# Optimization experiments

Measured on AMD Instinct MI355X. Metric: run time of the kernel, lower is better.

The kernel has to match this reference:

```python
import jax, jax.numpy as jnp
import numpy as np

D_MODEL = 1024
HEADS = 16
DEPTH = D_MODEL // HEADS
B, S = 4, 4096
EPS_K = 1e-6  # kernel feature epsilon
EPS_LN = 1e-6


def setup_inputs() -> dict:
    key = jax.random.key(0)
    ks = jax.random.split(key, 8)
    lecun = 1.0 / np.sqrt(D_MODEL)  # LecunNormal stddev
    glorot = np.sqrt(2.0 / (D_MODEL + D_MODEL))  # keras Dense default
    return {
        "q": jax.random.normal(ks[0], (B, S, D_MODEL), jnp.float32),
        "k": jax.random.normal(ks[1], (B, S, D_MODEL), jnp.float32),
        "v": jax.random.normal(ks[2], (B, S, D_MODEL), jnp.float32),
        "mask": jnp.ones((B, S), jnp.float32),
        "wq": jax.random.normal(ks[3], (D_MODEL, D_MODEL), jnp.float32) * lecun,
        "wk": jax.random.normal(ks[4], (D_MODEL, D_MODEL), jnp.float32) * lecun,
        "wv": jax.random.normal(ks[5], (D_MODEL, D_MODEL), jnp.float32) * lecun,
        "ln_gamma": jnp.ones((D_MODEL,), jnp.float32),
        "ln_beta": jnp.zeros((D_MODEL,), jnp.float32),
        "dense_w": jax.random.normal(ks[6], (D_MODEL, D_MODEL), jnp.float32) * glorot,
        "dense_b": jnp.zeros((D_MODEL,), jnp.float32),
    }


def _layernorm(x, g, b):
    m = jnp.mean(x, axis=-1, keepdims=True)
    var = jnp.var(x, axis=-1, keepdims=True)
    return (x - m) * jax.lax.rsqrt(var + EPS_LN) * g + b


def _split_heads(x):
    bsz, sl, _ = x.shape
    return x.reshape(bsz, sl, HEADS, DEPTH).transpose(0, 2, 1, 3)  # [B,H,S,depth]


def reference(q, k, v, mask, wq, wk, wv, ln_gamma, ln_beta, dense_w, dense_b):
    bsz = q.shape[0]
    em = mask[:, None, :, None]  # [B,1,S,1] broadcast over heads/depth
    qh = _split_heads(_layernorm(q @ wq, ln_gamma, ln_beta))
    kh = _split_heads(_layernorm(k @ wk, ln_gamma, ln_beta))
    vh = _split_heads(_layernorm(v @ wv, ln_gamma, ln_beta))
    q_prime = jax.nn.relu(qh) + EPS_K
    k_prime = (jax.nn.relu(kh) + EPS_K) * em
    vh = vh * em
    kv = jnp.einsum('bhnd,bhne->bhde', k_prime, vh)  # [B,H,depth,depth]
    z = 1.0 / (jnp.einsum('bhnd,bhd->bhn', q_prime, k_prime.sum(axis=-2)) + EPS_K)
    att = jnp.einsum('bhnd,bhde,bhn->bhne', q_prime, kv, z)  # [B,H,S,depth]
    # Faithful to original: reshape WITHOUT transposing heads back.
    att = att.reshape(bsz, -1, D_MODEL)  # [B,S,d_model]
    out = att @ dense_w + dense_b
    return _layernorm(out, ln_gamma, ln_beta)
```

## Files before the change

kernel.cpp:

```cpp
#include <hip/hip_runtime.h>
#include <hip/hip_bf16.h>
#include <stdint.h>

#define D_MODEL 1024
#define S_LEN   4096
#define BATCH   4
#define HEADS   16
#define DEPTH   64
#define ROWS    (BATCH*S_LEN)
#define EPS_K_F 1e-6f
#define EPS_LN_F 1e-6f

typedef __attribute__((ext_vector_type(8))) short short8;
typedef __attribute__((ext_vector_type(4))) float f32x4;

__device__ __forceinline__ unsigned short f2bf(float f) {
  union { float f; unsigned u; } x; x.f = f;
  unsigned r = x.u + 0x7FFF + ((x.u >> 16) & 1);
  return (unsigned short)(r >> 16);
}
__device__ __forceinline__ float bf2f(unsigned short b) {
  union { unsigned u; float f; } x; x.u = ((unsigned)b) << 16;
  return x.f;
}
__device__ __forceinline__ void gload16(const void* g, void* l) {
  __builtin_amdgcn_global_load_lds(
      (const __attribute__((address_space(1))) void*)g,
      (__attribute__((address_space(3))) void*)l, 16, 0, 0);
}

__global__ __launch_bounds__(256) void cvt_f32_bf16_k(
    const float* __restrict__ in, unsigned short* __restrict__ out, int n4) {
  int i = blockIdx.x * 256 + threadIdx.x;
  if (i < n4) {
    float4 v = ((const float4*)in)[i];
    ushort4 o;
    o.x = f2bf(v.x); o.y = f2bf(v.y); o.z = f2bf(v.z); o.w = f2bf(v.w);
    ((ushort4*)out)[i] = o;
  }
}

__global__ __launch_bounds__(256) void wtrans_k(
    const float* __restrict__ W, unsigned short* __restrict__ Wt) {
  __shared__ float tile[32][33];
  int n0 = blockIdx.x * 32, k0 = blockIdx.y * 32;
  int tx = threadIdx.x & 31, ty = threadIdx.x >> 5;
  #pragma unroll
  for (int i = 0; i < 32; i += 8)
    tile[ty + i][tx] = W[(size_t)(k0 + ty + i) * D_MODEL + n0 + tx];
  __syncthreads();
  #pragma unroll
  for (int i = 0; i < 32; i += 8)
    Wt[(size_t)(n0 + ty + i) * D_MODEL + k0 + tx] = f2bf(tile[tx][ty + i]);
}


#define GEMM_EPILOGUE(HASBIAS)                                               \
  if (HASBIAS) {                                                             \
    float bv[4];                                                             \
    _Pragma("unroll")                                                        \
    for (int n = 0; n < 4; ++n)                                              \
      bv[n] = bias[(int)n0 + wcn * 64 + n * 16 + l15];                       \
    _Pragma("unroll")                                                        \
    for (int m = 0; m < 8; ++m)                                              \
      _Pragma("unroll")                                                      \
      for (int n = 0; n < 4; ++n)                                            \
        _Pragma("unroll")                                                    \
        for (int j = 0; j < 4; ++j)                                          \
          acc[m][n][j] += bv[n];                                             \
  }                                                                          \
  int seg = (int)(n0 >> 6) + wcn;                                            \
  _Pragma("unroll")                                                          \
  for (int m = 0; m < 8; ++m) {                                              \
    float s[4], s2[4];                                                       \
    _Pragma("unroll")                                                        \
    for (int j = 0; j < 4; ++j) {                                            \
      float a = 0.f, b = 0.f;                                                \
      _Pragma("unroll")                                                      \
      for (int n = 0; n < 4; ++n) { float x = acc[m][n][j]; a += x; b += x*x; } \
      s[j] = a; s2[j] = b;                                                   \
    }                                                                        \
    _Pragma("unroll")                                                        \
    for (int off = 1; off < 16; off <<= 1) {                                 \
      _Pragma("unroll")                                                      \
      for (int j = 0; j < 4; ++j) {                                          \
        s[j]  += __shfl_xor(s[j],  off);                                     \
        s2[j] += __shfl_xor(s2[j], off);                                     \
      }                                                                      \
    }                                                                        \
    if (l15 == 0) {                                                          \
      _Pragma("unroll")                                                      \
      for (int j = 0; j < 4; ++j) {                                          \
        int rg = (int)m0 + wr * 128 + m * 16 + lhi * 4 + j;                  \
        psum[rg * 16 + seg] = s[j];                                          \
        psq [rg * 16 + seg] = s2[j];                                         \
      }                                                                      \
    }                                                                        \
  }                                                                          \
  _Pragma("unroll")                                                          \
  for (int m = 0; m < 8; ++m)                                                \
    _Pragma("unroll")                                                        \
    for (int j = 0; j < 4; ++j) {                                            \
      size_t row = m0 + wr * 128 + m * 16 + lhi * 4 + j;                     \
      _Pragma("unroll")                                                      \
      for (int n = 0; n < 4; ++n) {                                          \
        int col = (int)n0 + wcn * 64 + n * 16 + l15;                         \
        Cb[row * N + col] = f2bf(acc[m][n][j]);                              \
      }                                                                      \
    }

#define GEMM_COMPUTE_TILE(ABUF, BBUF)                                        \
  _Pragma("unroll")                                                          \
  for (int kk = 0; kk < 2; ++kk) {                                           \
    short8 bfr[4];                                                           \
    _Pragma("unroll")                                                        \
    for (int n = 0; n < 4; ++n) {                                            \
      int rr = wcn * 64 + n * 16 + l15;                                      \
      int cx = (kk * 4 + lhi) ^ (l15 & 7);                                   \
      bfr[n] = *(const short8*)&(BBUF)[rr * 64 + cx * 8];                    \
    }                                                                        \
    _Pragma("unroll")                                                        \
    for (int mh = 0; mh < 2; ++mh) {                                         \
      short8 af[4];                                                          \
      _Pragma("unroll")                                                      \
      for (int m = 0; m < 4; ++m) {                                          \
        int rr = wr * 128 + (mh * 4 + m) * 16 + l15;                         \
        int cx = (kk * 4 + lhi) ^ (l15 & 7);                                 \
        af[m] = *(const short8*)&(ABUF)[rr * 64 + cx * 8];                   \
      }                                                                      \
      asm volatile("s_waitcnt lgkmcnt(0)" ::: "memory");                     \
      __builtin_amdgcn_sched_barrier(0);                                     \
      __builtin_amdgcn_s_setprio(1);                                         \
      _Pragma("unroll")                                                      \
      for (int m = 0; m < 4; ++m)                                            \
        _Pragma("unroll")                                                    \
        for (int n = 0; n < 4; ++n)                                          \
          acc[mh * 4 + m][n] = __builtin_amdgcn_mfma_f32_16x16x32_bf16(      \
              af[m], bfr[n], acc[mh * 4 + m][n], 0, 0, 0);                   \
      __builtin_amdgcn_s_setprio(0);                                         \
    }                                                                        \
  }

__global__ __launch_bounds__(512, 2) void gemm_bt_k(
    const unsigned short* __restrict__ A,
    const unsigned short* __restrict__ Bt,
    unsigned short* __restrict__ Cb,
    float* __restrict__ psum, float* __restrict__ psq,
    const float* __restrict__ bias,
    const float* __restrict__ side_src,
    unsigned short* __restrict__ side_dst,
    int M, int N, int K) {
  __shared__ unsigned short Al[2][256 * 64];
  __shared__ unsigned short Bl[2][256 * 64];
  int t = threadIdx.x;
  int lane = t & 63, wid = t >> 6;
  int wr = wid >> 2, wcn = wid & 3;
  int l15 = lane & 15, lhi = lane >> 4;
  int p = blockIdx.x;
  int cb = (p >> 3) & 3;
  int rb = (p & 7) | ((p >> 5) << 3);
  size_t m0 = (size_t)rb * 256, n0 = (size_t)cb * 256;
  f32x4 acc[8][4] = {};

  const int KT = K >> 6;

#define STAGE_AB(kof_, buf_) do {                                            \
    _Pragma("unroll")                                                        \
    for (int sub = 0; sub < 4; ++sub) {                                      \
      int idx = sub * 512 + t; int r_ = idx >> 3, cl_ = idx & 7;             \
      int cg_ = cl_ ^ (r_ & 7);                                              \
      gload16(A + (m0 + r_) * (size_t)K + (kof_) + cg_ * 8,                  \
              &Al[buf_][idx * 8]);                                           \
    }                                                                        \
    _Pragma("unroll")                                                        \
    for (int sub = 0; sub < 4; ++sub) {                                      \
      int idx = sub * 512 + t; int r_ = idx >> 3, cl_ = idx & 7;             \
      int cg_ = cl_ ^ (r_ & 7);                                              \
      gload16(Bt + (n0 + r_) * (size_t)K + (kof_) + cg_ * 8,                 \
              &Bl[buf_][idx * 8]);                                           \
    }                                                                        \
  } while (0)

  float4 sreg0 = {}, sreg1 = {};
  size_t sbase = (size_t)p * 65536 + (size_t)t * 8;

  STAGE_AB(0, 0);
  if (side_dst) {
    sreg0 = *(const float4*)(side_src + sbase);
    sreg1 = *(const float4*)(side_src + sbase + 4);
  }
  asm volatile("s_waitcnt vmcnt(0)" ::: "memory");
  __builtin_amdgcn_s_barrier();
  __builtin_amdgcn_sched_barrier(0);

  for (int kt = 0; kt < KT; ++kt) {
    int buf = kt & 1;
    if (kt + 1 < KT) STAGE_AB((kt + 1) << 6, buf ^ 1);
    if (side_dst) {
      uint4 pk;
      pk.x = (unsigned)f2bf(sreg0.x) | ((unsigned)f2bf(sreg0.y) << 16);
      pk.y = (unsigned)f2bf(sreg0.z) | ((unsigned)f2bf(sreg0.w) << 16);
      pk.z = (unsigned)f2bf(sreg1.x) | ((unsigned)f2bf(sreg1.y) << 16);
      pk.w = (unsigned)f2bf(sreg1.z) | ((unsigned)f2bf(sreg1.w) << 16);
      *(uint4*)(side_dst + sbase + (size_t)kt * 4096) = pk;
      if (kt + 1 < KT) {
        const float* sp = side_src + sbase + (size_t)(kt + 1) * 4096;
        sreg0 = *(const float4*)sp;
        sreg1 = *(const float4*)(sp + 4);
      }
    }
    __builtin_amdgcn_sched_barrier(0);
    GEMM_COMPUTE_TILE(Al[buf], Bl[buf]);
    asm volatile("s_waitcnt vmcnt(0) lgkmcnt(0)" ::: "memory");
    __builtin_amdgcn_s_barrier();
    __builtin_amdgcn_sched_barrier(0);
  }
#undef STAGE_AB

  GEMM_EPILOGUE(bias != nullptr)
}

__global__ __launch_bounds__(256) void ln_act_k(
    const unsigned short* __restrict__ Cb,
    const float* __restrict__ psum, const float* __restrict__ psq,
    const float* __restrict__ gamma, const float* __restrict__ beta,
    const float* __restrict__ mask,
    unsigned short* __restrict__ out, int mode) {
  int row = blockIdx.x;
  int t = threadIdx.x;
  float s = 0.f, s2 = 0.f;
  #pragma unroll
  for (int i = 0; i < 16; ++i) { s += psum[row * 16 + i]; s2 += psq[row * 16 + i]; }
  float mean = s * (1.f / D_MODEL);
  float var = s2 * (1.f / D_MODEL) - mean * mean;
  float rstd = rsqrtf(var + EPS_LN_F);
  float mk = (mode > 0) ? mask[row] : 1.f;
  ushort4 cv = ((const ushort4*)(Cb + (size_t)row * D_MODEL))[t];
  float4 gv = ((const float4*)gamma)[t];
  float4 bv = ((const float4*)beta)[t];
  float av[4] = {bf2f(cv.x), bf2f(cv.y), bf2f(cv.z), bf2f(cv.w)};
  float g4[4] = {gv.x, gv.y, gv.z, gv.w};
  float b4[4] = {bv.x, bv.y, bv.z, bv.w};
  unsigned short ov[4];
  #pragma unroll
  for (int j = 0; j < 4; ++j) {
    float ln = (av[j] - mean) * rstd * g4[j] + b4[j];
    if (mode == 0)      ln = fmaxf(ln, 0.f) + EPS_K_F;
    else if (mode == 1) ln = (fmaxf(ln, 0.f) + EPS_K_F) * mk;
    else                ln = ln * mk;
    ov[j] = f2bf(ln);
  }
  ushort4 o; o.x = ov[0]; o.y = ov[1]; o.z = ov[2]; o.w = ov[3];
  ((ushort4*)(out + (size_t)row * D_MODEL))[t] = o;
}

__global__ __launch_bounds__(256) void ln_final_k(
    const unsigned short* __restrict__ Cb,
    const float* __restrict__ psum, const float* __restrict__ psq,
    const float* __restrict__ gamma, const float* __restrict__ beta,
    float* __restrict__ out) {
  int row = blockIdx.x;
  int t = threadIdx.x;
  float s = 0.f, s2 = 0.f;
  #pragma unroll
  for (int i = 0; i < 16; ++i) { s += psum[row * 16 + i]; s2 += psq[row * 16 + i]; }
  float mean = s * (1.f / D_MODEL);
  float var = s2 * (1.f / D_MODEL) - mean * mean;
  float rstd = rsqrtf(var + EPS_LN_F);
  ushort4 cv = ((const ushort4*)(Cb + (size_t)row * D_MODEL))[t];
  float4 gv = ((const float4*)gamma)[t];
  float4 bv = ((const float4*)beta)[t];
  float4 w;
  w.x = (bf2f(cv.x) - mean) * rstd * gv.x + bv.x;
  w.y = (bf2f(cv.y) - mean) * rstd * gv.y + bv.y;
  w.z = (bf2f(cv.z) - mean) * rstd * gv.z + bv.z;
  w.w = (bf2f(cv.w) - mean) * rstd * gv.w + bv.w;
  ((float4*)(out + (size_t)row * D_MODEL))[t] = w;
}

__global__ __launch_bounds__(256) void kv_mfma_k(
    const unsigned short* __restrict__ Kp, const unsigned short* __restrict__ Vp,
    float* __restrict__ part, float* __restrict__ kspart) {
  __shared__ unsigned short Kl[4096];
  __shared__ unsigned short Vl[4096];
  int bh = blockIdx.y, chunk = blockIdx.x;
  int b_ = bh >> 4, h = bh & 15;
  int t = threadIdx.x, lane = t & 63, w = t >> 6;
  int l15 = lane & 15, g = lane >> 4;

  int sn = t >> 2, sd16 = t & 3;
  int sc = sd16 ^ ((sn >> 3) & 3);
  size_t goff = (size_t)sn * D_MODEL + h * DEPTH + sd16 * 16;
  int ldst = sn * 64 + sc * 16;

  short8 ones;
  #pragma unroll
  for (int i = 0; i < 8; ++i) ones[i] = (short)0x3F80;

  f32x4 acc[4] = {};
  f32x4 ks = {};

  int baseA = ((w ^ g) << 4) + l15;
  int baseB0 = ((0 ^ g) << 4) + l15;
  int baseB1 = ((1 ^ g) << 4) + l15;
  int baseB2 = ((2 ^ g) << 4) + l15;
  int baseB3 = ((3 ^ g) << 4) + l15;

  size_t rowbase = ((size_t)b_ * S_LEN + (size_t)chunk * 512) * D_MODEL;
  for (int tile = 0; tile < 8; ++tile) {
    const unsigned short* kg = Kp + rowbase + (size_t)tile * 64 * D_MODEL + goff;
    const unsigned short* vg = Vp + rowbase + (size_t)tile * 64 * D_MODEL + goff;
    uint4 ra = *(const uint4*)kg;
    uint4 rb = *(const uint4*)(kg + 8);
    uint4 rc = *(const uint4*)vg;
    uint4 rd = *(const uint4*)(vg + 8);
    __syncthreads();
    *(uint4*)&Kl[ldst]     = ra;
    *(uint4*)&Kl[ldst + 8] = rb;
    *(uint4*)&Vl[ldst]     = rc;
    *(uint4*)&Vl[ldst + 8] = rd;
    __syncthreads();
    #pragma unroll
    for (int kk = 0; kk < 2; ++kk) {
      int nb = (kk * 32 + g * 8) * 64;
      short8 af, bf0, bf1, bf2, bf3;
      #pragma unroll
      for (int i = 0; i < 8; ++i) {
        int rowoff = nb + i * 64;
        af[i]  = (short)Kl[rowoff + baseA];
        bf0[i] = (short)Vl[rowoff + baseB0];
        bf1[i] = (short)Vl[rowoff + baseB1];
        bf2[i] = (short)Vl[rowoff + baseB2];
        bf3[i] = (short)Vl[rowoff + baseB3];
      }
      acc[0] = __builtin_amdgcn_mfma_f32_16x16x32_bf16(af, bf0, acc[0], 0, 0, 0);
      acc[1] = __builtin_amdgcn_mfma_f32_16x16x32_bf16(af, bf1, acc[1], 0, 0, 0);
      acc[2] = __builtin_amdgcn_mfma_f32_16x16x32_bf16(af, bf2, acc[2], 0, 0, 0);
      acc[3] = __builtin_amdgcn_mfma_f32_16x16x32_bf16(af, bf3, acc[3], 0, 0, 0);
      ks     = __builtin_amdgcn_mfma_f32_16x16x32_bf16(af, ones, ks, 0, 0, 0);
    }
  }
  float* pp = part + ((size_t)bh * 8 + chunk) * 4096;
  #pragma unroll
  for (int nf = 0; nf < 4; ++nf)
    #pragma unroll
    for (int r = 0; r < 4; ++r)
      pp[(16 * w + 4 * g + r) * 64 + 16 * nf + l15] = acc[nf][r];
  if (l15 == 0) {
    #pragma unroll
    for (int r = 0; r < 4; ++r)
      kspart[((size_t)bh * 8 + chunk) * 64 + 16 * w + 4 * g + r] = ks[r];
  }
}

__global__ __launch_bounds__(256) void kv_reduce_k(
    const float* __restrict__ part, const float* __restrict__ kspart,
    unsigned short* __restrict__ KVT, float* __restrict__ ksum) {
  int bh = blockIdx.x, t = threadIdx.x;
  for (int idx = t; idx < 4096; idx += 256) {
    int d = idx >> 6, e = idx & 63;
    float s = 0.f;
    #pragma unroll
    for (int c = 0; c < 8; ++c)
      s += part[((size_t)bh * 8 + c) * 4096 + d * 64 + e];
    KVT[(size_t)bh * 4096 + e * 64 + d] = f2bf(s);
  }
  if (t < 64) {
    float s = 0.f;
    #pragma unroll
    for (int c = 0; c < 8; ++c) s += kspart[((size_t)bh * 8 + c) * 64 + t];
    ksum[bh * 64 + t] = s;
  }
}

__global__ __launch_bounds__(256) void att_k(
    const unsigned short* __restrict__ Qp, const unsigned short* __restrict__ KVT,
    const float* __restrict__ ksum, unsigned short* __restrict__ att) {
  __shared__ unsigned short Ql[128 * 64];
  __shared__ unsigned short Kl[64 * 64];
  __shared__ float ksl[64];
  __shared__ float zl[128];
  int bh = blockIdx.y;
  int b = bh >> 4, h = bh & 15;
  int r0 = blockIdx.x * 128;
  int t = threadIdx.x, lane = t & 63, wid = t >> 6;
  int l15 = lane & 15, lhi = lane >> 4;
  #pragma unroll
  for (int i = 0; i < 4; ++i) {
    int cid = i * 256 + t;
    int r = cid >> 3, c8 = cid & 7;
    gload16(Qp + ((size_t)(b * S_LEN + r0 + r)) * D_MODEL + h * DEPTH + c8 * 8,
            &Ql[cid * 8]);
  }
  #pragma unroll
  for (int i = 0; i < 2; ++i) {
    int cid = i * 256 + t;
    gload16(KVT + (size_t)bh * 4096 + cid * 8, &Kl[cid * 8]);
  }
  if (t < 64) ksl[t] = ksum[bh * 64 + t];
  asm volatile("s_waitcnt vmcnt(0)" ::: "memory");
  __syncthreads();
  {
    int r = t >> 1, half = t & 1;
    float s = 0.f;
    #pragma unroll
    for (int j = 0; j < 32; ++j)
      s += bf2f(Ql[r * 64 + half * 32 + j]) * ksl[half * 32 + j];
    s += __shfl_xor(s, 1);
    if (half == 0) zl[r] = 1.f / (s + EPS_K_F);
  }
  __syncthreads();
  f32x4 acc[2][4] = {};
  #pragma unroll
  for (int kk = 0; kk < 2; ++kk) {
    short8 af[2], bfr[4];
    #pragma unroll
    for (int m = 0; m < 2; ++m)
      af[m] = *(const short8*)&Ql[(wid * 32 + m * 16 + l15) * 64 + kk * 32 + lhi * 8];
    #pragma unroll
    for (int n = 0; n < 4; ++n)
      bfr[n] = *(const short8*)&Kl[(n * 16 + l15) * 64 + kk * 32 + lhi * 8];
    #pragma unroll
    for (int m = 0; m < 2; ++m)
      #pragma unroll
      for (int n = 0; n < 4; ++n)
        acc[m][n] = __builtin_amdgcn_mfma_f32_16x16x32_bf16(af[m], bfr[n], acc[m][n], 0, 0, 0);
  }
  #pragma unroll
  for (int m = 0; m < 2; ++m)
    #pragma unroll
    for (int j = 0; j < 4; ++j) {
      int rl = wid * 32 + m * 16 + lhi * 4 + j;
      int n = r0 + rl;
      float z = zl[rl];
      #pragma unroll
      for (int nf = 0; nf < 4; ++nf) {
        int ee = nf * 16 + l15;
        size_t orow = (size_t)b * S_LEN + h * 256 + (n >> 4);
        int ocol = (n & 15) * 64 + ee;
        att[orow * D_MODEL + ocol] = f2bf(acc[m][nf][j] * z);
      }
    }
}

extern "C" void kernel_launch(void* const* d_in, const int* in_sizes, int n_in,
                              void* d_out, int out_size, void* d_ws, size_t ws_size,
                              hipStream_t stream) {
  (void)in_sizes; (void)n_in; (void)out_size; (void)ws_size;
  const float* q     = (const float*)d_in[0];
  const float* k     = (const float*)d_in[1];
  const float* v     = (const float*)d_in[2];
  const float* mask  = (const float*)d_in[3];
  const float* wq    = (const float*)d_in[4];
  const float* wk    = (const float*)d_in[5];
  const float* wv    = (const float*)d_in[6];
  const float* gamma = (const float*)d_in[7];
  const float* beta  = (const float*)d_in[8];
  const float* dw    = (const float*)d_in[9];
  const float* db    = (const float*)d_in[10];
  float* out = (float*)d_out;

  char* ws = (char*)d_ws;
  unsigned short* bufA = (unsigned short*)(ws);
  unsigned short* Qp   = (unsigned short*)(ws + 33554432);
  unsigned short* bufB = (unsigned short*)(ws + 67108864);
  unsigned short* Kp   = bufB;
  unsigned short* Vp   = (unsigned short*)(ws + 100663296);
  unsigned short* WqT  = (unsigned short*)(ws + 134217728);
  unsigned short* WkT = WqT + 1048576;
  unsigned short* WvT = WkT + 1048576;
  unsigned short* WdT = WvT + 1048576;
  float* part   = (float*)(ws);
  float* kspart = (float*)(ws + 8388608);
  unsigned short* KVT = (unsigned short*)(ws + 142606336);
  float* ksum = (float*)(ws + 143130624);
  float* psum = (float*)(ws + 143654912);
  float* psq  = (float*)(ws + 144703488);
  unsigned short* Cqkv = (unsigned short*)d_out;
  unsigned short* Cd   = Qp;

  dim3 b256(256);
  dim3 b512(512);
  int n4 = ROWS * D_MODEL / 4;
  dim3 cvtg(n4 / 256);
  dim3 wtg(32, 32);
  dim3 gemmg(256);
  dim3 lng(ROWS);

  wtrans_k<<<wtg, b256, 0, stream>>>(wq, WqT);
  wtrans_k<<<wtg, b256, 0, stream>>>(wk, WkT);
  wtrans_k<<<wtg, b256, 0, stream>>>(wv, WvT);
  wtrans_k<<<wtg, b256, 0, stream>>>(dw, WdT);

  cvt_f32_bf16_k<<<cvtg, b256, 0, stream>>>(q, bufA, n4);

  gemm_bt_k<<<gemmg, b512, 0, stream>>>(bufA, WqT, Cqkv, psum, psq, nullptr,
                                        k, bufB, ROWS, D_MODEL, D_MODEL);
  ln_act_k<<<lng, b256, 0, stream>>>(Cqkv, psum, psq, gamma, beta, nullptr, Qp, 0);

  gemm_bt_k<<<gemmg, b512, 0, stream>>>(bufB, WkT, Cqkv, psum, psq, nullptr,
                                        v, bufA, ROWS, D_MODEL, D_MODEL);
  ln_act_k<<<lng, b256, 0, stream>>>(Cqkv, psum, psq, gamma, beta, mask, Kp, 1);

  gemm_bt_k<<<gemmg, b512, 0, stream>>>(bufA, WvT, Cqkv, psum, psq, nullptr,
                                        nullptr, nullptr, ROWS, D_MODEL, D_MODEL);
  ln_act_k<<<lng, b256, 0, stream>>>(Cqkv, psum, psq, gamma, beta, mask, Vp, 2);

  kv_mfma_k<<<dim3(8, 64), b256, 0, stream>>>(Kp, Vp, part, kspart);
  kv_reduce_k<<<dim3(64), b256, 0, stream>>>(part, kspart, KVT, ksum);
  att_k<<<dim3(32, 64), b256, 0, stream>>>(Qp, KVT, ksum, bufA);

  gemm_bt_k<<<gemmg, b512, 0, stream>>>(bufA, WdT, Cd, psum, psq, db,
                                        nullptr, nullptr, ROWS, D_MODEL, D_MODEL);
  ln_final_k<<<lng, b256, 0, stream>>>(Cd, psum, psq, gamma, beta, out);
}
```

Baseline: 352.5 us.

## Replace double-buffered LDS staging with single buffer in GEMM kernel

```diff
diff --git a/kernel.cpp b/kernel.cpp
--- a/kernel.cpp
+++ b/kernel.cpp
@@ -150,8 +150,8 @@
     const float* __restrict__ side_src,
     unsigned short* __restrict__ side_dst,
     int M, int N, int K) {
-  __shared__ unsigned short Al[2][256 * 64];
-  __shared__ unsigned short Bl[2][256 * 64];
+  __shared__ unsigned short Al[256 * 64];
+  __shared__ unsigned short Bl[256 * 64];
   int t = threadIdx.x;
   int lane = t & 63, wid = t >> 6;
   int wr = wid >> 2, wcn = wid & 3;
@@ -164,58 +164,55 @@
 
   const int KT = K >> 6;
 
-#define STAGE_AB(kof_, buf_) do {                                            \
+#define STAGE_AB(kof_) do {                                                  \
     _Pragma("unroll")                                                        \
     for (int sub = 0; sub < 4; ++sub) {                                      \
       int idx = sub * 512 + t; int r_ = idx >> 3, cl_ = idx & 7;             \
       int cg_ = cl_ ^ (r_ & 7);                                              \
-      gload16(A + (m0 + r_) * (size_t)K + (kof_) + cg_ * 8,                  \
-              &Al[buf_][idx * 8]);                                           \
+      gload16(A + (m0 + r_) * (size_t)K + (kof_) + cg_ * 8, &Al[idx * 8]);   \
     }                                                                        \
     _Pragma("unroll")                                                        \
     for (int sub = 0; sub < 4; ++sub) {                                      \
       int idx = sub * 512 + t; int r_ = idx >> 3, cl_ = idx & 7;             \
       int cg_ = cl_ ^ (r_ & 7);                                              \
-      gload16(Bt + (n0 + r_) * (size_t)K + (kof_) + cg_ * 8,                 \
-              &Bl[buf_][idx * 8]);                                           \
+      gload16(Bt + (n0 + r_) * (size_t)K + (kof_) + cg_ * 8, &Bl[idx * 8]);  \
     }                                                                        \
   } while (0)
 
   float4 sreg0 = {}, sreg1 = {};
   size_t sbase = (size_t)p * 65536 + (size_t)t * 8;
 
-  STAGE_AB(0, 0);
-  if (side_dst) {
-    sreg0 = *(const float4*)(side_src + sbase);
-    sreg1 = *(const float4*)(side_src + sbase + 4);
-  }
-  asm volatile("s_waitcnt vmcnt(0)" ::: "memory");
-  __builtin_amdgcn_s_barrier();
-  __builtin_amdgcn_sched_barrier(0);
-
   for (int kt = 0; kt < KT; ++kt) {
-    int buf = kt & 1;
-    if (kt + 1 < KT) STAGE_AB((kt + 1) << 6, buf ^ 1);
+    STAGE_AB(kt << 6);
     if (side_dst) {
-      uint4 pk;
-      pk.x = (unsigned)f2bf(sreg0.x) | ((unsigned)f2bf(sreg0.y) << 16);
-      pk.y = (unsigned)f2bf(sreg0.z) | ((unsigned)f2bf(sreg0.w) << 16);
-      pk.z = (unsigned)f2bf(sreg1.x) | ((unsigned)f2bf(sreg1.y) << 16);
-      pk.w = (unsigned)f2bf(sreg1.z) | ((unsigned)f2bf(sreg1.w) << 16);
-      *(uint4*)(side_dst + sbase + (size_t)kt * 4096) = pk;
-      if (kt + 1 < KT) {
-        const float* sp = side_src + sbase + (size_t)(kt + 1) * 4096;
-        sreg0 = *(const float4*)sp;
-        sreg1 = *(const float4*)(sp + 4);
+      if (kt > 0) {
+        uint4 pk;
+        pk.x = (unsigned)f2bf(sreg0.x) | ((unsigned)f2bf(sreg0.y) << 16);
+        pk.y = (unsigned)f2bf(sreg0.z) | ((unsigned)f2bf(sreg0.w) << 16);
+        pk.z = (unsigned)f2bf(sreg1.x) | ((unsigned)f2bf(sreg1.y) << 16);
+        pk.w = (unsigned)f2bf(sreg1.z) | ((unsigned)f2bf(sreg1.w) << 16);
+        *(uint4*)(side_dst + sbase + (size_t)(kt - 1) * 4096) = pk;
       }
+      const float* sp = side_src + sbase + (size_t)kt * 4096;
+      sreg0 = *(const float4*)sp;
+      sreg1 = *(const float4*)(sp + 4);
     }
-    __builtin_amdgcn_sched_barrier(0);
-    GEMM_COMPUTE_TILE(Al[buf], Bl[buf]);
-    asm volatile("s_waitcnt vmcnt(0) lgkmcnt(0)" ::: "memory");
+    asm volatile("s_waitcnt vmcnt(0)" ::: "memory");
     __builtin_amdgcn_s_barrier();
     __builtin_amdgcn_sched_barrier(0);
+    GEMM_COMPUTE_TILE(Al, Bl);
+    __builtin_amdgcn_s_barrier();
+    __builtin_amdgcn_sched_barrier(0);
   }
 #undef STAGE_AB
+  if (side_dst) {
+    uint4 pk;
+    pk.x = (unsigned)f2bf(sreg0.x) | ((unsigned)f2bf(sreg0.y) << 16);
+    pk.y = (unsigned)f2bf(sreg0.z) | ((unsigned)f2bf(sreg0.w) << 16);
+    pk.z = (unsigned)f2bf(sreg1.x) | ((unsigned)f2bf(sreg1.y) << 16);
+    pk.w = (unsigned)f2bf(sreg1.z) | ((unsigned)f2bf(sreg1.w) << 16);
+    *(uint4*)(side_dst + sbase + (size_t)(KT - 1) * 4096) = pk;
+  }
 
   GEMM_EPILOGUE(bias != nullptr)
 }
```

Measured after the change: 366.2 us. 1.04x slower.

## Restructure GEMM mainloop into half-K stages with deeper prefetch; batch input conversions

Applied to the files above, without the earlier changes.

```diff
diff --git a/kernel.cpp b/kernel.cpp
--- a/kernel.cpp
+++ b/kernel.cpp
@@ -29,15 +29,19 @@
       (__attribute__((address_space(3))) void*)l, 16, 0, 0);
 }
 
-__global__ __launch_bounds__(256) void cvt_f32_bf16_k(
-    const float* __restrict__ in, unsigned short* __restrict__ out, int n4) {
-  int i = blockIdx.x * 256 + threadIdx.x;
-  if (i < n4) {
-    float4 v = ((const float4*)in)[i];
-    ushort4 o;
-    o.x = f2bf(v.x); o.y = f2bf(v.y); o.z = f2bf(v.z); o.w = f2bf(v.w);
-    ((ushort4*)out)[i] = o;
-  }
+__global__ __launch_bounds__(256) void cvt3_k(
+    const float* __restrict__ q, const float* __restrict__ k,
+    const float* __restrict__ v,
+    unsigned short* __restrict__ xq, unsigned short* __restrict__ xk,
+    unsigned short* __restrict__ xv, int nb_per) {
+  int tb = blockIdx.x / nb_per;
+  int i = (blockIdx.x % nb_per) * 256 + threadIdx.x;
+  const float* src = (tb == 0) ? q : (tb == 1) ? k : v;
+  unsigned short* dst = (tb == 0) ? xq : (tb == 1) ? xk : xv;
+  float4 val = ((const float4*)src)[i];
+  ushort4 o;
+  o.x = f2bf(val.x); o.y = f2bf(val.y); o.z = f2bf(val.z); o.w = f2bf(val.w);
+  ((ushort4*)dst)[i] = o;
 }
 
 __global__ __launch_bounds__(256) void wtrans_k(
@@ -109,37 +113,47 @@
       }                                                                      \
     }
 
-#define GEMM_COMPUTE_TILE(ABUF, BBUF)                                        \
-  _Pragma("unroll")                                                          \
-  for (int kk = 0; kk < 2; ++kk) {                                           \
-    short8 bfr[4];                                                           \
+#define STAGE_HALF(kof_, slot_, h_) do {                                     \
+    _Pragma("unroll")                                                        \
+    for (int j = 0; j < 2; ++j) {                                            \
+      int idx = j * 512 + t; int r_ = idx >> 2; int cs_ = idx & 3;           \
+      int c_ = cs_ ^ (r_ & 3);                                               \
+      gload16(A + (m0 + r_) * (size_t)K + (kof_) + (h_) * 32 + c_ * 8,       \
+              &Al[slot_][(h_) * 8192 + idx * 8]);                            \
+    }                                                                        \
+    _Pragma("unroll")                                                        \
+    for (int j = 0; j < 2; ++j) {                                            \
+      int idx = j * 512 + t; int r_ = idx >> 2; int cs_ = idx & 3;           \
+      int c_ = cs_ ^ (r_ & 3);                                               \
+      gload16(Bt + (n0 + r_) * (size_t)K + (kof_) + (h_) * 32 + c_ * 8,      \
+              &Bl[slot_][(h_) * 8192 + idx * 8]);                            \
+    }                                                                        \
+  } while (0)
+
+#define PH_READ_B(kk_)                                                       \
     _Pragma("unroll")                                                        \
     for (int n = 0; n < 4; ++n) {                                            \
-      int rr = wcn * 64 + n * 16 + l15;                                      \
-      int cx = (kk * 4 + lhi) ^ (l15 & 7);                                   \
-      bfr[n] = *(const short8*)&(BBUF)[rr * 64 + cx * 8];                    \
-    }                                                                        \
-    _Pragma("unroll")                                                        \
-    for (int mh = 0; mh < 2; ++mh) {                                         \
-      short8 af[4];                                                          \
+      int rb_ = wcn * 64 + n * 16 + l15;                                     \
+      bfr[n] = *(const short8*)&Bl[slot][(kk_) * 8192 + rb_ * 32 + cswz];    \
+    }
+#define PH_READ_A(kk_, mh_)                                                  \
+    _Pragma("unroll")                                                        \
+    for (int m = 0; m < 4; ++m) {                                            \
+      int ra_ = wr * 128 + ((mh_) * 4 + m) * 16 + l15;                       \
+      af[m] = *(const short8*)&Al[slot][(kk_) * 8192 + ra_ * 32 + cswz];     \
+    }
+#define PH_MFMA(mh_)                                                         \
+    __builtin_amdgcn_s_setprio(1);                                           \
+    _Pragma("unroll")                                                        \
+    for (int m = 0; m < 4; ++m)                                              \
       _Pragma("unroll")                                                      \
-      for (int m = 0; m < 4; ++m) {                                          \
-        int rr = wr * 128 + (mh * 4 + m) * 16 + l15;                         \
-        int cx = (kk * 4 + lhi) ^ (l15 & 7);                                 \
-        af[m] = *(const short8*)&(ABUF)[rr * 64 + cx * 8];                   \
-      }                                                                      \
-      asm volatile("s_waitcnt lgkmcnt(0)" ::: "memory");                     \
-      __builtin_amdgcn_sched_barrier(0);                                     \
-      __builtin_amdgcn_s_setprio(1);                                         \
-      _Pragma("unroll")                                                      \
-      for (int m = 0; m < 4; ++m)                                            \
-        _Pragma("unroll")                                                    \
-        for (int n = 0; n < 4; ++n)                                          \
-          acc[mh * 4 + m][n] = __builtin_amdgcn_mfma_f32_16x16x32_bf16(      \
-              af[m], bfr[n], acc[mh * 4 + m][n], 0, 0, 0);                   \
-      __builtin_amdgcn_s_setprio(0);                                         \
-    }                                                                        \
-  }
+      for (int n = 0; n < 4; ++n)                                            \
+        acc[(mh_) * 4 + m][n] = __builtin_amdgcn_mfma_f32_16x16x32_bf16(     \
+            af[m], bfr[n], acc[(mh_) * 4 + m][n], 0, 0, 0);                  \
+    __builtin_amdgcn_s_setprio(0);
+#define LGKM0                                                                \
+    asm volatile("s_waitcnt lgkmcnt(0)" ::: "memory");                       \
+    __builtin_amdgcn_sched_barrier(0);
 
 __global__ __launch_bounds__(512, 2) void gemm_bt_k(
     const unsigned short* __restrict__ A,
@@ -147,15 +161,14 @@
     unsigned short* __restrict__ Cb,
     float* __restrict__ psum, float* __restrict__ psq,
     const float* __restrict__ bias,
-    const float* __restrict__ side_src,
-    unsigned short* __restrict__ side_dst,
     int M, int N, int K) {
-  __shared__ unsigned short Al[2][256 * 64];
-  __shared__ unsigned short Bl[2][256 * 64];
+  __shared__ unsigned short Al[2][16384];
+  __shared__ unsigned short Bl[2][16384];
   int t = threadIdx.x;
   int lane = t & 63, wid = t >> 6;
   int wr = wid >> 2, wcn = wid & 3;
   int l15 = lane & 15, lhi = lane >> 4;
+  const int cswz = (lhi ^ (l15 & 3)) << 3;
   int p = blockIdx.x;
   int cb = (p >> 3) & 3;
   int rb = (p & 7) | ((p >> 5) << 3);
@@ -164,58 +177,46 @@
 
   const int KT = K >> 6;
 
-#define STAGE_AB(kof_, buf_) do {                                            \
-    _Pragma("unroll")                                                        \
-    for (int sub = 0; sub < 4; ++sub) {                                      \
-      int idx = sub * 512 + t; int r_ = idx >> 3, cl_ = idx & 7;             \
-      int cg_ = cl_ ^ (r_ & 7);                                              \
-      gload16(A + (m0 + r_) * (size_t)K + (kof_) + cg_ * 8,                  \
-              &Al[buf_][idx * 8]);                                           \
-    }                                                                        \
-    _Pragma("unroll")                                                        \
-    for (int sub = 0; sub < 4; ++sub) {                                      \
-      int idx = sub * 512 + t; int r_ = idx >> 3, cl_ = idx & 7;             \
-      int cg_ = cl_ ^ (r_ & 7);                                              \
-      gload16(Bt + (n0 + r_) * (size_t)K + (kof_) + cg_ * 8,                 \
-              &Bl[buf_][idx * 8]);                                           \
-    }                                                                        \
-  } while (0)
-
-  float4 sreg0 = {}, sreg1 = {};
-  size_t sbase = (size_t)p * 65536 + (size_t)t * 8;
-
-  STAGE_AB(0, 0);
-  if (side_dst) {
-    sreg0 = *(const float4*)(side_src + sbase);
-    sreg1 = *(const float4*)(side_src + sbase + 4);
-  }
-  asm volatile("s_waitcnt vmcnt(0)" ::: "memory");
+  STAGE_HALF(0, 0, 0);  STAGE_HALF(0, 0, 1);
+  STAGE_HALF(64, 1, 0); STAGE_HALF(64, 1, 1);
+  asm volatile("s_waitcnt vmcnt(8)" ::: "memory");
   __builtin_amdgcn_s_barrier();
   __builtin_amdgcn_sched_barrier(0);
 
   for (int kt = 0; kt < KT; ++kt) {
-    int buf = kt & 1;
-    if (kt + 1 < KT) STAGE_AB((kt + 1) << 6, buf ^ 1);
-    if (side_dst) {
-      uint4 pk;
-      pk.x = (unsigned)f2bf(sreg0.x) | ((unsigned)f2bf(sreg0.y) << 16);
-      pk.y = (unsigned)f2bf(sreg0.z) | ((unsigned)f2bf(sreg0.w) << 16);
-      pk.z = (unsigned)f2bf(sreg1.x) | ((unsigned)f2bf(sreg1.y) << 16);
-      pk.w = (unsigned)f2bf(sreg1.z) | ((unsigned)f2bf(sreg1.w) << 16);
-      *(uint4*)(side_dst + sbase + (size_t)kt * 4096) = pk;
-      if (kt + 1 < KT) {
-        const float* sp = side_src + sbase + (size_t)(kt + 1) * 4096;
-        sreg0 = *(const float4*)sp;
-        sreg1 = *(const float4*)(sp + 4);
-      }
-    }
-    __builtin_amdgcn_sched_barrier(0);
-    GEMM_COMPUTE_TILE(Al[buf], Bl[buf]);
-    asm volatile("s_waitcnt vmcnt(0) lgkmcnt(0)" ::: "memory");
+    const int slot = kt & 1;
+    short8 af[4], bfr[4];
+    PH_READ_B(0)
+    PH_READ_A(0, 0)
+    LGKM0
+    PH_MFMA(0)
+    PH_READ_A(0, 1)
+    LGKM0
     __builtin_amdgcn_s_barrier();
     __builtin_amdgcn_sched_barrier(0);
-  }
-#undef STAGE_AB
+    if (kt + 2 < KT) STAGE_HALF((kt + 2) << 6, slot, 0);
+    __builtin_amdgcn_sched_barrier(0);
+    PH_MFMA(1)
+    PH_READ_B(1)
+    PH_READ_A(1, 0)
+    LGKM0
+    PH_MFMA(0)
+    PH_READ_A(1, 1)
+    LGKM0
+    __builtin_amdgcn_s_barrier();
+    __builtin_amdgcn_sched_barrier(0);
+    if (kt + 2 < KT) STAGE_HALF((kt + 2) << 6, slot, 1);
+    __builtin_amdgcn_sched_barrier(0);
+    PH_MFMA(1)
+    if (kt + 1 < KT) {
+      if (kt + 2 < KT)
+        asm volatile("s_waitcnt vmcnt(8)" ::: "memory");
+      else
+        asm volatile("s_waitcnt vmcnt(0)" ::: "memory");
+      __builtin_amdgcn_s_barrier();
+      __builtin_amdgcn_sched_barrier(0);
+    }
+  }
 
   GEMM_EPILOGUE(bias != nullptr)
 }
@@ -461,28 +462,29 @@
   float* out = (float*)d_out;
 
   char* ws = (char*)d_ws;
-  unsigned short* bufA = (unsigned short*)(ws);
-  unsigned short* Qp   = (unsigned short*)(ws + 33554432);
-  unsigned short* bufB = (unsigned short*)(ws + 67108864);
-  unsigned short* Kp   = bufB;
-  unsigned short* Vp   = (unsigned short*)(ws + 100663296);
-  unsigned short* WqT  = (unsigned short*)(ws + 134217728);
+  unsigned short* Xq  = (unsigned short*)(ws);
+  unsigned short* Xk  = (unsigned short*)(ws + 33554432);
+  unsigned short* Xv  = (unsigned short*)(ws + 67108864);
+  unsigned short* Qp  = Xq;
+  unsigned short* Kp  = Xk;
+  unsigned short* Vp  = Xv;
+  unsigned short* Cd  = Xq;
+  unsigned short* WqT = (unsigned short*)(ws + 100663296);
   unsigned short* WkT = WqT + 1048576;
   unsigned short* WvT = WkT + 1048576;
   unsigned short* WdT = WvT + 1048576;
-  float* part   = (float*)(ws);
-  float* kspart = (float*)(ws + 8388608);
-  unsigned short* KVT = (unsigned short*)(ws + 142606336);
-  float* ksum = (float*)(ws + 143130624);
-  float* psum = (float*)(ws + 143654912);
-  float* psq  = (float*)(ws + 144703488);
+  float* part   = (float*)(ws + 109051904);
+  float* kspart = (float*)(ws + 117440512);
+  unsigned short* KVT = (unsigned short*)(ws + 117964800);
+  float* ksum = (float*)(ws + 118489088);
+  float* psum = (float*)(ws + 119537664);
+  float* psq  = (float*)(ws + 120586240);
   unsigned short* Cqkv = (unsigned short*)d_out;
-  unsigned short* Cd   = Qp;
 
   dim3 b256(256);
   dim3 b512(512);
   int n4 = ROWS * D_MODEL / 4;
-  dim3 cvtg(n4 / 256);
+  int nb_per = n4 / 256;
   dim3 wtg(32, 32);
   dim3 gemmg(256);
   dim3 lng(ROWS);
@@ -492,25 +494,25 @@
   wtrans_k<<<wtg, b256, 0, stream>>>(wv, WvT);
   wtrans_k<<<wtg, b256, 0, stream>>>(dw, WdT);
 
-  cvt_f32_bf16_k<<<cvtg, b256, 0, stream>>>(q, bufA, n4);
-
-  gemm_bt_k<<<gemmg, b512, 0, stream>>>(bufA, WqT, Cqkv, psum, psq, nullptr,
-                                        k, bufB, ROWS, D_MODEL, D_MODEL);
+  cvt3_k<<<dim3(3 * nb_per), b256, 0, stream>>>(q, k, v, Xq, Xk, Xv, nb_per);
+
+  gemm_bt_k<<<gemmg, b512, 0, stream>>>(Xq, WqT, Cqkv, psum, psq, nullptr,
+                                        ROWS, D_MODEL, D_MODEL);
   ln_act_k<<<lng, b256, 0, stream>>>(Cqkv, psum, psq, gamma, beta, nullptr, Qp, 0);
 
-  gemm_bt_k<<<gemmg, b512, 0, stream>>>(bufB, WkT, Cqkv, psum, psq, nullptr,
-                                        v, bufA, ROWS, D_MODEL, D_MODEL);
+  gemm_bt_k<<<gemmg, b512, 0, stream>>>(Xk, WkT, Cqkv, psum, psq, nullptr,
+                                        ROWS, D_MODEL, D_MODEL);
   ln_act_k<<<lng, b256, 0, stream>>>(Cqkv, psum, psq, gamma, beta, mask, Kp, 1);
 
-  gemm_bt_k<<<gemmg, b512, 0, stream>>>(bufA, WvT, Cqkv, psum, psq, nullptr,
-                                        nullptr, nullptr, ROWS, D_MODEL, D_MODEL);
+  gemm_bt_k<<<gemmg, b512, 0, stream>>>(Xv, WvT, Cqkv, psum, psq, nullptr,
+                                        ROWS, D_MODEL, D_MODEL);
   ln_act_k<<<lng, b256, 0, stream>>>(Cqkv, psum, psq, gamma, beta, mask, Vp, 2);
 
   kv_mfma_k<<<dim3(8, 64), b256, 0, stream>>>(Kp, Vp, part, kspart);
   kv_reduce_k<<<dim3(64), b256, 0, stream>>>(part, kspart, KVT, ksum);
-  att_k<<<dim3(32, 64), b256, 0, stream>>>(Qp, KVT, ksum, bufA);
-
-  gemm_bt_k<<<gemmg, b512, 0, stream>>>(bufA, WdT, Cd, psum, psq, db,
-                                        nullptr, nullptr, ROWS, D_MODEL, D_MODEL);
+  att_k<<<dim3(32, 64), b256, 0, stream>>>(Qp, KVT, ksum, Cqkv);
+
+  gemm_bt_k<<<gemmg, b512, 0, stream>>>(Cqkv, WdT, Cd, psum, psq, db,
+                                        ROWS, D_MODEL, D_MODEL);
   ln_final_k<<<lng, b256, 0, stream>>>(Cd, psum, psq, gamma, beta, out);
 }
```

After: 360.5 us. 1.02x slower.
